# Kernel tuning notes

Hardware: AMD Instinct MI355X
Metric: run time of the kernel (lower is better)

## Reference

```python
import jax, jax.numpy as jnp
import numpy as np

B, N, C, K = 8, 4096, 128, 16
POOL_RATE = 4  # npoint = N // POOL_RATE


def setup_inputs() -> dict:
    key = jax.random.key(0)
    k1, k2, k3 = jax.random.split(key, 3)
    vertices = jax.random.normal(k1, (B, 3, N), dtype=jnp.float32)
    feature_map = jax.random.normal(k2, (B, C, N), dtype=jnp.float32)
    # pre-flattened global knn indices, values in [0, B*N) as produced upstream
    idx = jax.random.randint(k3, (B * N * K,), 0, B * N, dtype=jnp.int64)
    return {"vertices": vertices, "feature_map": feature_map, "idx": idx}


def farthest_point_sample(xyz, npoint):
    """xyz: (B, N, 3) -> centroid indices (B, npoint).
    Deterministic start at index 0 (torch version uses a random start)."""
    b, n, _ = xyz.shape

    def step(carry, _):
        distance, farthest = carry
        centroid = jnp.take_along_axis(xyz, farthest[:, None, None], axis=1)  # (B,1,3)
        dist = jnp.sum((xyz - centroid) ** 2, axis=-1)  # (B,N)
        distance = jnp.minimum(distance, dist)
        new_farthest = jnp.argmax(distance, axis=-1)
        return (distance, new_farthest), farthest

    dist0 = jnp.full((b, n), 1e10, dtype=xyz.dtype)
    far0 = jnp.zeros((b,), dtype=jnp.int32)
    _, cents = jax.lax.scan(step, (dist0, far0), None, length=npoint)
    return cents.T  # (B, npoint)


def reference(vertices, feature_map, idx):
    b, c, n = feature_map.shape
    # get_graph_feature with precomputed flat idx: gather neighbors then max-pool
    flat = feature_map.transpose(0, 2, 1).reshape(b * n, c)        # (B*N, C)
    neigh = flat[idx].reshape(b, n, K, c)                          # (B,N,K,C)
    pooled = jnp.max(neigh, axis=2)                                # (B,N,C) == (B,C,N) pooled_feature, channel-last

    npoint = n // POOL_RATE
    xyz = vertices.transpose(0, 2, 1)                              # (B,N,3)
    cents = farthest_point_sample(xyz, npoint)                     # (B,npoint)

    vertices_pool = jnp.take_along_axis(xyz, cents[:, :, None], axis=1).transpose(0, 2, 1)     # (B,3,npoint)
    feature_map_pool = jnp.take_along_axis(pooled, cents[:, :, None], axis=1).transpose(0, 2, 1)  # (B,C,npoint)
    return (vertices_pool, feature_map_pool)
```

## Files before the change

### kernel.cpp

```cpp
#include <hip/hip_runtime.h>
#include <hip/hip_bf16.h>
#include <math.h>

#define B_SZ 8
#define N_SZ 4096
#define C_SZ 128
#define K_SZ 16
#define NPOINT 1024

#define FPS_T 512
#define FPS_PAIRS 4

typedef float vf2 __attribute__((ext_vector_type(2)));

template <int CTRL>
__device__ __forceinline__ unsigned long long dpp_kmax_step(unsigned long long k) {
    const unsigned lo = (unsigned)k;
    const unsigned hi = (unsigned)(k >> 32);
    const unsigned lo2 = (unsigned)__builtin_amdgcn_update_dpp(0, (int)lo, CTRL, 0xF, 0xF, true);
    const unsigned hi2 = (unsigned)__builtin_amdgcn_update_dpp(0, (int)hi, CTRL, 0xF, 0xF, true);
    const unsigned long long k2 = ((unsigned long long)hi2 << 32) | (unsigned long long)lo2;
    return (k2 > k) ? k2 : k;
}
__device__ __forceinline__ unsigned long long wave_kmax63(unsigned long long k) {
    k = dpp_kmax_step<0x111>(k);
    k = dpp_kmax_step<0x112>(k);
    k = dpp_kmax_step<0x114>(k);
    k = dpp_kmax_step<0x118>(k);
    k = dpp_kmax_step<0x142>(k);
    k = dpp_kmax_step<0x143>(k);
    return k;
}
__device__ __forceinline__ unsigned long long kmax2(unsigned long long a,
                                                   unsigned long long b) {
    return a > b ? a : b;
}

__global__ void transpose_fm(const float* __restrict__ fm, float* __restrict__ fmT) {
    __shared__ float tile[32][33];
    const int b  = blockIdx.z;
    const int c0 = blockIdx.y * 32;
    const int n0 = blockIdx.x * 32;
    const int tx = threadIdx.x;
    const int ty = threadIdx.y;
    const float* p = fm + (size_t)b * C_SZ * N_SZ;
#pragma unroll
    for (int i = 0; i < 4; i++) {
        tile[ty + i * 8][tx] = p[(size_t)(c0 + ty + i * 8) * N_SZ + n0 + tx];
    }
    __syncthreads();
    float* q = fmT + (size_t)b * N_SZ * C_SZ;
#pragma unroll
    for (int i = 0; i < 4; i++) {
        q[(size_t)(n0 + ty + i * 8) * C_SZ + c0 + tx] = tile[tx][ty + i * 8];
    }
}

__global__ __launch_bounds__(FPS_T) void fps_kernel(
        const float* __restrict__ verts,
        float* __restrict__ out_vp,
        int* __restrict__ cents)
{
#pragma clang fp contract(off)
#pragma clang fp reassociate(off)
    __shared__ float4 sp[N_SZ];
    __shared__ int    scent[NPOINT];
    __shared__ alignas(16) unsigned long long ckey[2][8];

    const int b    = blockIdx.x;
    const int tid  = threadIdx.x;
    const int lane = tid & 63;
    const int wid  = tid >> 6;
    const float* vb = verts + (size_t)b * 3 * N_SZ;

    vf2 px[FPS_PAIRS], py[FPS_PAIRS], pz[FPS_PAIRS], dd[FPS_PAIRS];
#pragma unroll
    for (int p = 0; p < FPS_PAIRS; p++) {
        const int n0 = tid + (2 * p) * FPS_T;
        const int n1 = n0 + FPS_T;
        const float x0 = vb[n0],            x1 = vb[n1];
        const float y0 = vb[N_SZ + n0],     y1 = vb[N_SZ + n1];
        const float z0 = vb[2 * N_SZ + n0], z1 = vb[2 * N_SZ + n1];
        px[p] = (vf2){x0, x1};
        py[p] = (vf2){y0, y1};
        pz[p] = (vf2){z0, z1};
        dd[p] = (vf2){1e10f, 1e10f};
        sp[n0] = make_float4(x0, y0, z0, 0.0f);
        sp[n1] = make_float4(x1, y1, z1, 0.0f);
    }
    __syncthreads();

    int ci = 0;
    float4 c0 = sp[0];
    float cx = c0.x, cy = c0.y, cz = c0.z;

    for (int i = 0; i < NPOINT; i++) {
        if (tid == 0) scent[i] = ci;

        const vf2 cx2 = (vf2){cx, cx};
        const vf2 cy2 = (vf2){cy, cy};
        const vf2 cz2 = (vf2){cz, cz};

        float bv = -1.0f;
        int   bj = 0;
#pragma unroll
        for (int p = 0; p < FPS_PAIRS; p++) {
            const vf2 dx = px[p] - cx2;
            const vf2 dy = py[p] - cy2;
            const vf2 dz = pz[p] - cz2;
            vf2 s = dx * dx + dy * dy;
            s = s + dz * dz;
            vf2 d;
            d.x = fminf(dd[p].x, s.x);
            d.y = fminf(dd[p].y, s.y);
            dd[p] = d;
            if (d.x > bv) { bv = d.x; bj = 2 * p; }
            if (d.y > bv) { bv = d.y; bj = 2 * p + 1; }
        }
        const unsigned n = (unsigned)(tid + (bj << 9));
        unsigned long long key =
            ((unsigned long long)__float_as_uint(bv) << 32) |
            (unsigned long long)(4095u - n);

        key = wave_kmax63(key);
        const int par = i & 1;
        if (lane == 63) ckey[par][wid] = key;
        __syncthreads();

        const ulonglong2* kb = (const ulonglong2*)(&ckey[par][0]);
        const ulonglong2 a0 = kb[0], a1 = kb[1], a2 = kb[2], a3 = kb[3];
        const unsigned long long m0 = kmax2(a0.x, a0.y);
        const unsigned long long m1 = kmax2(a1.x, a1.y);
        const unsigned long long m2 = kmax2(a2.x, a2.y);
        const unsigned long long m3 = kmax2(a3.x, a3.y);
        const unsigned long long kk = kmax2(kmax2(m0, m1), kmax2(m2, m3));

        ci = (int)(4095u - (unsigned)kk);
        const float4 c = sp[ci];
        cx = c.x; cy = c.y; cz = c.z;
    }
    __syncthreads();

    for (int i = tid; i < NPOINT; i += FPS_T) {
        const int cc = scent[i];
        const float4 v = sp[cc];
        cents[b * NPOINT + i] = cc;
        out_vp[(b * 3 + 0) * NPOINT + i] = v.x;
        out_vp[(b * 3 + 1) * NPOINT + i] = v.y;
        out_vp[(b * 3 + 2) * NPOINT + i] = v.z;
    }
}

#define GT_J 16
__global__ __launch_bounds__(1024) void pool_gather_t(
        const float* __restrict__ fmT,
        const int* __restrict__ idx,
        const int* __restrict__ cents,
        float* __restrict__ out_fp)
{
    __shared__ float tile[C_SZ][GT_J + 1];
    const int tid  = threadIdx.x;
    const int lane = tid & 63;
    const int w    = tid >> 6;
    const int j0   = blockIdx.x * GT_J;
    const int gp   = j0 + w;
    const int b    = gp >> 10;
    const int ci   = cents[gp];
    const int* ip  = idx + ((size_t)(b * N_SZ + ci)) * K_SZ;
    const float2* src = (const float2*)fmT;

    float2 acc = make_float2(-INFINITY, -INFINITY);
#pragma unroll
    for (int k = 0; k < K_SZ; k++) {
        const int p = ip[k];
        const float2 v = src[(size_t)p * (C_SZ / 2) + lane];
        acc.x = fmaxf(acc.x, v.x);
        acc.y = fmaxf(acc.y, v.y);
    }
    tile[2 * lane][w]     = acc.x;
    tile[2 * lane + 1][w] = acc.y;
    __syncthreads();

    float* q = out_fp + (size_t)b * C_SZ * NPOINT + (j0 & (NPOINT - 1));
#pragma unroll
    for (int it = 0; it < 2; it++) {
        const int e  = tid + it * 1024;
        const int c  = e >> 4;
        const int jj = e & (GT_J - 1);
        q[(size_t)c * NPOINT + jj] = tile[c][jj];
    }
}

extern "C" void kernel_launch(void* const* d_in, const int* in_sizes, int n_in,
                              void* d_out, int out_size, void* d_ws, size_t ws_size,
                              hipStream_t stream) {
    const float* verts = (const float*)d_in[0];
    const float* fm    = (const float*)d_in[1];
    const int*   idx   = (const int*)d_in[2];

    float* out    = (float*)d_out;
    float* out_vp = out;
    float* out_fp = out + (size_t)B_SZ * 3 * NPOINT;

    char* ws = (char*)d_ws;
    float* fmT   = (float*)ws;
    int*   cents = (int*)(ws + (size_t)B_SZ * N_SZ * C_SZ * 4);

    dim3 tb(32, 8);
    transpose_fm<<<dim3(N_SZ / 32, C_SZ / 32, B_SZ), tb, 0, stream>>>(fm, fmT);
    fps_kernel<<<B_SZ, FPS_T, 0, stream>>>(verts, out_vp, cents);
    pool_gather_t<<<(B_SZ * NPOINT) / GT_J, 1024, 0, stream>>>(fmT, idx, cents, out_fp);
}
```

Measured before the change: 698.1 us.

## Fuse transpose into FPS launch and reduce argmax via shared atomicMin

Merges the feature-map transpose into the FPS kernel as extra blocks, so the transpose runs on idle CUs while the eight serial FPS blocks iterate, and one kernel launch is removed. The per-iteration cross-wave argmax now uses an inverted key, a DPP min-reduction and an LDS atomicMin into a rotating four-entry slot, replacing the per-wave key store followed by an 8-way read and reduce. This shortens the serial critical path of each FPS step. The trade-off is that the fused transpose blocks may contend with the FPS blocks for CU resources, and the tie-breaking and DPP bound_ctrl semantics changed.

```diff
diff --git a/kernel.cpp b/kernel.cpp
--- a/kernel.cpp
+++ b/kernel.cpp
@@ -10,54 +10,33 @@
 
 #define FPS_T 512
 #define FPS_PAIRS 4
+#define TR_BLOCKS 2048
 
 typedef float vf2 __attribute__((ext_vector_type(2)));
 
 template <int CTRL>
-__device__ __forceinline__ unsigned long long dpp_kmax_step(unsigned long long k) {
-    const unsigned lo = (unsigned)k;
-    const unsigned hi = (unsigned)(k >> 32);
-    const unsigned lo2 = (unsigned)__builtin_amdgcn_update_dpp(0, (int)lo, CTRL, 0xF, 0xF, true);
-    const unsigned hi2 = (unsigned)__builtin_amdgcn_update_dpp(0, (int)hi, CTRL, 0xF, 0xF, true);
+__device__ __forceinline__ unsigned long long dpp_kmin_step(unsigned long long k) {
+    const int lo = (int)(unsigned)k;
+    const int hi = (int)(unsigned)(k >> 32);
+    const unsigned lo2 = (unsigned)__builtin_amdgcn_update_dpp(lo, lo, CTRL, 0xF, 0xF, false);
+    const unsigned hi2 = (unsigned)__builtin_amdgcn_update_dpp(hi, hi, CTRL, 0xF, 0xF, false);
     const unsigned long long k2 = ((unsigned long long)hi2 << 32) | (unsigned long long)lo2;
-    return (k2 > k) ? k2 : k;
-}
-__device__ __forceinline__ unsigned long long wave_kmax63(unsigned long long k) {
-    k = dpp_kmax_step<0x111>(k);
-    k = dpp_kmax_step<0x112>(k);
-    k = dpp_kmax_step<0x114>(k);
-    k = dpp_kmax_step<0x118>(k);
-    k = dpp_kmax_step<0x142>(k);
-    k = dpp_kmax_step<0x143>(k);
+    return (k2 < k) ? k2 : k;
+}
+__device__ __forceinline__ unsigned long long wave_kmin63(unsigned long long k) {
+    k = dpp_kmin_step<0x111>(k);
+    k = dpp_kmin_step<0x112>(k);
+    k = dpp_kmin_step<0x114>(k);
+    k = dpp_kmin_step<0x118>(k);
+    k = dpp_kmin_step<0x142>(k);
+    k = dpp_kmin_step<0x143>(k);
     return k;
 }
-__device__ __forceinline__ unsigned long long kmax2(unsigned long long a,
-                                                   unsigned long long b) {
-    return a > b ? a : b;
-}
-
-__global__ void transpose_fm(const float* __restrict__ fm, float* __restrict__ fmT) {
-    __shared__ float tile[32][33];
-    const int b  = blockIdx.z;
-    const int c0 = blockIdx.y * 32;
-    const int n0 = blockIdx.x * 32;
-    const int tx = threadIdx.x;
-    const int ty = threadIdx.y;
-    const float* p = fm + (size_t)b * C_SZ * N_SZ;
-#pragma unroll
-    for (int i = 0; i < 4; i++) {
-        tile[ty + i * 8][tx] = p[(size_t)(c0 + ty + i * 8) * N_SZ + n0 + tx];
-    }
-    __syncthreads();
-    float* q = fmT + (size_t)b * N_SZ * C_SZ;
-#pragma unroll
-    for (int i = 0; i < 4; i++) {
-        q[(size_t)(n0 + ty + i * 8) * C_SZ + c0 + tx] = tile[tx][ty + i * 8];
-    }
-}
-
-__global__ __launch_bounds__(FPS_T) void fps_kernel(
+
+__global__ __launch_bounds__(FPS_T) void fps_fused(
         const float* __restrict__ verts,
+        const float* __restrict__ fm,
+        float* __restrict__ fmT,
         float* __restrict__ out_vp,
         int* __restrict__ cents)
 {
@@ -65,12 +44,38 @@
 #pragma clang fp reassociate(off)
     __shared__ float4 sp[N_SZ];
     __shared__ int    scent[NPOINT];
-    __shared__ alignas(16) unsigned long long ckey[2][8];
+    __shared__ unsigned long long slot[4];
+
+    const int tid = threadIdx.x;
+
+    if (blockIdx.x >= B_SZ) {
+        float* tile = (float*)sp;
+        const int half = tid >> 8;
+        const int t    = tid & 255;
+        const int tx   = t & 31;
+        const int ty   = t >> 5;
+        const int g    = 2 * (blockIdx.x - B_SZ) + half;
+        const int b    = g >> 9;
+        const int r    = g & 511;
+        const int n0   = (r & 127) * 32;
+        const int c0   = (r >> 7) * 32;
+        float* tl = tile + half * (32 * 33);
+        const float* p = fm + (size_t)b * C_SZ * N_SZ;
+#pragma unroll
+        for (int i = 0; i < 4; i++) {
+            tl[(ty + i * 8) * 33 + tx] = p[(size_t)(c0 + ty + i * 8) * N_SZ + n0 + tx];
+        }
+        __syncthreads();
+        float* q = fmT + (size_t)b * N_SZ * C_SZ;
+#pragma unroll
+        for (int i = 0; i < 4; i++) {
+            q[(size_t)(n0 + ty + i * 8) * C_SZ + c0 + tx] = tl[tx * 33 + ty + i * 8];
+        }
+        return;
+    }
 
     const int b    = blockIdx.x;
-    const int tid  = threadIdx.x;
     const int lane = tid & 63;
-    const int wid  = tid >> 6;
     const float* vb = verts + (size_t)b * 3 * N_SZ;
 
     vf2 px[FPS_PAIRS], py[FPS_PAIRS], pz[FPS_PAIRS], dd[FPS_PAIRS];
@@ -88,6 +93,7 @@
         sp[n0] = make_float4(x0, y0, z0, 0.0f);
         sp[n1] = make_float4(x1, y1, z1, 0.0f);
     }
+    if (tid < 4) slot[tid] = ~0ull;
     __syncthreads();
 
     int ci = 0;
@@ -119,23 +125,16 @@
         }
         const unsigned n = (unsigned)(tid + (bj << 9));
         unsigned long long key =
-            ((unsigned long long)__float_as_uint(bv) << 32) |
-            (unsigned long long)(4095u - n);
-
-        key = wave_kmax63(key);
-        const int par = i & 1;
-        if (lane == 63) ckey[par][wid] = key;
+            ((unsigned long long)(~__float_as_uint(bv)) << 32) |
+            (unsigned long long)n;
+
+        key = wave_kmin63(key);
+        if (lane == 63) atomicMin(&slot[i & 3], key);
+        if (tid == 0)   slot[(i + 2) & 3] = ~0ull;
         __syncthreads();
 
-        const ulonglong2* kb = (const ulonglong2*)(&ckey[par][0]);
-        const ulonglong2 a0 = kb[0], a1 = kb[1], a2 = kb[2], a3 = kb[3];
-        const unsigned long long m0 = kmax2(a0.x, a0.y);
-        const unsigned long long m1 = kmax2(a1.x, a1.y);
-        const unsigned long long m2 = kmax2(a2.x, a2.y);
-        const unsigned long long m3 = kmax2(a3.x, a3.y);
-        const unsigned long long kk = kmax2(kmax2(m0, m1), kmax2(m2, m3));
-
-        ci = (int)(4095u - (unsigned)kk);
+        const unsigned long long kk = slot[i & 3];
+        ci = (int)(unsigned)kk;
         const float4 c = sp[ci];
         cx = c.x; cy = c.y; cz = c.z;
     }
@@ -206,8 +205,6 @@
     float* fmT   = (float*)ws;
     int*   cents = (int*)(ws + (size_t)B_SZ * N_SZ * C_SZ * 4);
 
-    dim3 tb(32, 8);
-    transpose_fm<<<dim3(N_SZ / 32, C_SZ / 32, B_SZ), tb, 0, stream>>>(fm, fmT);
-    fps_kernel<<<B_SZ, FPS_T, 0, stream>>>(verts, out_vp, cents);
+    fps_fused<<<B_SZ + TR_BLOCKS, FPS_T, 0, stream>>>(verts, fm, fmT, out_vp, cents);
     pool_gather_t<<<(B_SZ * NPOINT) / GT_J, 1024, 0, stream>>>(fmT, idx, cents, out_fp);
 }
```

Result: slower. 817.0 us (+17.0%).

## Halve FPS block size and reduce argmax keys with double-precision max

Applied to the files above, without the earlier changes.

The farthest-point-sampling kernel now uses 256 threads with 16 points per thread instead of 512 threads with 8, which cuts the cross-wave reduction from 8 to 4 waves. The packed (distance, index) key is reinterpreted as a double so each DPP reduction step uses a single fmax on 64-bit floats instead of a 64-bit integer compare-and-select. The per-thread argmax is split into a branch-free max pass followed by an index-recovery scan. Each thread does twice the serial work per iteration, and the double-max ordering relies on the distances being non-negative so the bit patterns compare correctly.

```diff
diff --git a/kernel.cpp b/kernel.cpp
--- a/kernel.cpp
+++ b/kernel.cpp
@@ -8,32 +8,30 @@
 #define K_SZ 16
 #define NPOINT 1024
 
-#define FPS_T 512
-#define FPS_PAIRS 4
+#define FPS_T 256
+#define FPS_PAIRS 8
 
 typedef float vf2 __attribute__((ext_vector_type(2)));
 
 template <int CTRL>
-__device__ __forceinline__ unsigned long long dpp_kmax_step(unsigned long long k) {
-    const unsigned lo = (unsigned)k;
-    const unsigned hi = (unsigned)(k >> 32);
-    const unsigned lo2 = (unsigned)__builtin_amdgcn_update_dpp(0, (int)lo, CTRL, 0xF, 0xF, true);
-    const unsigned hi2 = (unsigned)__builtin_amdgcn_update_dpp(0, (int)hi, CTRL, 0xF, 0xF, true);
-    const unsigned long long k2 = ((unsigned long long)hi2 << 32) | (unsigned long long)lo2;
-    return (k2 > k) ? k2 : k;
-}
-__device__ __forceinline__ unsigned long long wave_kmax63(unsigned long long k) {
-    k = dpp_kmax_step<0x111>(k);
-    k = dpp_kmax_step<0x112>(k);
-    k = dpp_kmax_step<0x114>(k);
-    k = dpp_kmax_step<0x118>(k);
-    k = dpp_kmax_step<0x142>(k);
-    k = dpp_kmax_step<0x143>(k);
+__device__ __forceinline__ double dpp_dmax_step(double k) {
+    const unsigned long long u = __builtin_bit_cast(unsigned long long, k);
+    const int lo = (int)(unsigned)u;
+    const int hi = (int)(unsigned)(u >> 32);
+    const unsigned lo2 = (unsigned)__builtin_amdgcn_update_dpp(0, lo, CTRL, 0xF, 0xF, true);
+    const unsigned hi2 = (unsigned)__builtin_amdgcn_update_dpp(0, hi, CTRL, 0xF, 0xF, true);
+    const double k2 = __builtin_bit_cast(double,
+        ((unsigned long long)hi2 << 32) | (unsigned long long)lo2);
+    return fmax(k, k2);
+}
+__device__ __forceinline__ double wave_dmax63(double k) {
+    k = dpp_dmax_step<0x111>(k);
+    k = dpp_dmax_step<0x112>(k);
+    k = dpp_dmax_step<0x114>(k);
+    k = dpp_dmax_step<0x118>(k);
+    k = dpp_dmax_step<0x142>(k);
+    k = dpp_dmax_step<0x143>(k);
     return k;
-}
-__device__ __forceinline__ unsigned long long kmax2(unsigned long long a,
-                                                   unsigned long long b) {
-    return a > b ? a : b;
 }
 
 __global__ void transpose_fm(const float* __restrict__ fm, float* __restrict__ fmT) {
@@ -65,7 +63,7 @@
 #pragma clang fp reassociate(off)
     __shared__ float4 sp[N_SZ];
     __shared__ int    scent[NPOINT];
-    __shared__ alignas(16) unsigned long long ckey[2][8];
+    __shared__ alignas(16) double ckey[2][4];
 
     const int b    = blockIdx.x;
     const int tid  = threadIdx.x;
@@ -101,8 +99,7 @@
         const vf2 cy2 = (vf2){cy, cy};
         const vf2 cz2 = (vf2){cz, cz};
 
-        float bv = -1.0f;
-        int   bj = 0;
+        float m0 = -1.0f, m1 = -1.0f;
 #pragma unroll
         for (int p = 0; p < FPS_PAIRS; p++) {
             const vf2 dx = px[p] - cx2;
@@ -114,28 +111,33 @@
             d.x = fminf(dd[p].x, s.x);
             d.y = fminf(dd[p].y, s.y);
             dd[p] = d;
-            if (d.x > bv) { bv = d.x; bj = 2 * p; }
-            if (d.y > bv) { bv = d.y; bj = 2 * p + 1; }
+            m0 = fmaxf(m0, d.x);
+            m1 = fmaxf(m1, d.y);
         }
-        const unsigned n = (unsigned)(tid + (bj << 9));
-        unsigned long long key =
+        const float bv = fmaxf(m0, m1);
+
+        int bj = 0;
+#pragma unroll
+        for (int j = 15; j >= 0; j--) {
+            const float v = (j & 1) ? dd[j >> 1].y : dd[j >> 1].x;
+            if (v == bv) bj = j;
+        }
+
+        const unsigned n = (unsigned)(tid + (bj << 8));
+        double key = __builtin_bit_cast(double,
             ((unsigned long long)__float_as_uint(bv) << 32) |
-            (unsigned long long)(4095u - n);
-
-        key = wave_kmax63(key);
+            (unsigned long long)(4095u - n));
+
+        key = wave_dmax63(key);
         const int par = i & 1;
         if (lane == 63) ckey[par][wid] = key;
         __syncthreads();
 
-        const ulonglong2* kb = (const ulonglong2*)(&ckey[par][0]);
-        const ulonglong2 a0 = kb[0], a1 = kb[1], a2 = kb[2], a3 = kb[3];
-        const unsigned long long m0 = kmax2(a0.x, a0.y);
-        const unsigned long long m1 = kmax2(a1.x, a1.y);
-        const unsigned long long m2 = kmax2(a2.x, a2.y);
-        const unsigned long long m3 = kmax2(a3.x, a3.y);
-        const unsigned long long kk = kmax2(kmax2(m0, m1), kmax2(m2, m3));
-
-        ci = (int)(4095u - (unsigned)kk);
+        const double2* kb = (const double2*)(&ckey[par][0]);
+        const double2 k01 = kb[0], k23 = kb[1];
+        const double kk = fmax(fmax(k01.x, k01.y), fmax(k23.x, k23.y));
+
+        ci = (int)(4095u - (unsigned)__builtin_bit_cast(unsigned long long, kk));
         const float4 c = sp[ci];
         cx = c.x; cy = c.y; cz = c.z;
     }
```

Measured after the change: 643.5 us. 7.8% less time.
